# Kernel tuning notes

Measured on AMD Instinct MI355X. Metric: run time of the kernel, lower is better.

## Reference

```python
import jax, jax.numpy as jnp
import numpy as np

N, D, DR, DA = 50000, 128, 64, 64
R, A = 2000, 5000
L, H = 2, 2
E, E2, EA = 400000, 800000, 400000


def setup_inputs() -> dict:
    key = jax.random.key(0)
    ks = jax.random.split(key, 8)
    rng = np.random.default_rng(0)

    ee = np.stack([rng.integers(0, N, E), rng.integers(0, N, E)], 1)
    ee = ee[np.lexsort((ee[:, 1], ee[:, 0]))]            # sorted unique-ish ent-ent edges
    seg_id = np.repeat(np.arange(E), 2)                  # 2 relation rows per edge
    er_rel = rng.integers(0, R, E2)
    er_index = np.stack([np.repeat(ee[:, 0], 2), er_rel], 1)   # (node, rel) pairs
    ea_index = np.stack([rng.integers(0, N, EA), rng.integers(0, A, EA)], 1)
    ea_index = ea_index[np.lexsort((ea_index[:, 1], ea_index[:, 0]))]

    s192 = 1.0 / np.sqrt(192.0)
    s320 = 1.0 / np.sqrt(320.0)
    return {
        "ent_emb": jax.random.normal(ks[0], (N, D), jnp.float32) * 0.1,
        "rel_emb": jax.random.normal(ks[1], (R, DR), jnp.float32) * 0.1,
        "attr_emb": jax.random.normal(ks[2], (A, DA), jnp.float32) * 0.1,
        "w_r": jax.random.normal(ks[3], (192, 1), jnp.float32) * s192,
        "b_r": jnp.zeros((1,), jnp.float32),
        "w_a": jax.random.normal(ks[4], (192, 1), jnp.float32) * s192,
        "b_a": jnp.zeros((1,), jnp.float32),
        "ent_attn_w": jax.random.normal(ks[5], (L, H, 192, 1), jnp.float32) * s192,
        "ent_attn_b": jnp.zeros((L, H, 1), jnp.float32),
        "con_attn_w": jax.random.normal(ks[6], (L, H, 320, 1), jnp.float32) * s320,
        "con_attn_b": jnp.zeros((L, H, 1), jnp.float32),
        "ee_index": jnp.asarray(ee, jnp.int32),
        "seg_id": jnp.asarray(seg_id, jnp.int32),
        "er_rel": jnp.asarray(er_rel, jnp.int32),
        "er_index": jnp.asarray(er_index, jnp.int32),
        "ea_index": jnp.asarray(ea_index, jnp.int32),
    }


def _leaky(v):
    return jnp.where(v > 0, v, 0.3 * v)  # LeakyReLU(alpha=0.3)


def _seg_softmax(vals, seg, n):
    m = jax.ops.segment_max(vals, seg, num_segments=n)
    e = jnp.exp(vals - m[seg])
    s = jax.ops.segment_sum(e, seg, num_segments=n)
    return e / s[seg]


def _forward(ent_emb, rel_emb, attr_emb, w_r, b_r, w_a, b_a,
             eaw, eab, caw, cab, ee_index, seg_id, er_rel, er_index, ea_index):
    n, d = ent_emb.shape
    nl, nh = eaw.shape[0], eaw.shape[1]
    dh = d // nh
    ne = ee_index.shape[0]

    def concept(idx, emb, w, b):
        feat = jnp.concatenate([ent_emb[idx[:, 0]], emb[idx[:, 1]]], axis=1)
        a = _leaky(feat @ w + b).reshape(-1)
        p = _seg_softmax(a, idx[:, 0], n)                      # tf.sparse.softmax per row
        return jax.nn.relu(jax.ops.segment_sum(p[:, None] * emb[idx[:, 1]], idx[:, 0], num_segments=n))

    concept_rel = concept(er_index, rel_emb, w_r, b_r)         # (N, DR)
    concept_attr = concept(ea_index, attr_emb, w_a, b_a)       # (N, DA)

    row, col = ee_index[:, 0], ee_index[:, 1]
    # softmax over all-ones sparse adj == neighbor mean
    deg = jax.ops.segment_sum(jnp.ones((ne,), ent_emb.dtype), row, num_segments=n)
    x = jax.ops.segment_sum(ent_emb[col], row, num_segments=n) / jnp.maximum(deg, 1.0)[:, None]

    # segment_mean of relation embeddings over duplicate (h,t) edges
    cnt = jax.ops.segment_sum(jnp.ones((er_rel.shape[0],), ent_emb.dtype), seg_id, num_segments=ne)
    rels_mean = jax.ops.segment_sum(rel_emb[er_rel], seg_id, num_segments=ne) / jnp.maximum(cnt, 1.0)[:, None]

    # concept features per edge (same for every layer/head -> hoisted)
    con_feat = jnp.concatenate([concept_rel[row], concept_attr[row], rels_mean,
                                concept_rel[col], concept_attr[col]], axis=1)  # (E, 320)

    layer_outs = []
    for l in range(nl):
        x = jax.nn.relu(x)
        heads = x.reshape(n, nh, dh)
        outs = []
        for h in range(nh):
            xe = heads[:, h, :]
            nf = xe[col]
            ef = jnp.concatenate([xe[row], rels_mean, nf], axis=1)      # (E, 192)
            ea = _leaky(ef @ eaw[l, h] + eab[l, h]).reshape(-1)
            ca = _leaky(con_feat @ caw[l, h] + cab[l, h]).reshape(-1)
            p = jax.nn.softmax(ea * ca)         # tf.nn.softmax over all edge values
            p = _seg_softmax(p, row, n)          # then tf.sparse.softmax per row
            outs.append(jax.ops.segment_sum(p[:, None] * nf, row, num_segments=n))
        x = jnp.tanh(jnp.concatenate(outs, axis=1))
        layer_outs.append(x)

    grat_out = jnp.concatenate(layer_outs, axis=1)                     # (N, L*D)
    ent_out = jnp.concatenate([grat_out, concept_rel, concept_attr], axis=1)
    conc = jnp.concatenate([concept_rel, concept_attr], axis=1)
    return ent_out, conc


def reference(ent_emb, rel_emb, attr_emb, w_r, b_r, w_a, b_a,
              ent_attn_w, ent_attn_b, con_attn_w, con_attn_b,
              ee_index, seg_id, er_rel, er_index, ea_index):
    return _forward(ent_emb, rel_emb, attr_emb, w_r, b_r, w_a, b_a,
                    ent_attn_w, ent_attn_b, con_attn_w, con_attn_b,
                    ee_index, seg_id, er_rel, er_index, ea_index)
```

## Files before the change

### kernel.cpp

```cpp
#include <hip/hip_runtime.h>
#include <math.h>

#define NENT 50000
#define RREL 2000
#define AATT 5000
#define EE   400000
#define E2   800000
#define EAE  400000
#define PB   2048

__device__ __forceinline__ float leaky(float v){ return v > 0.f ? v : 0.3f * v; }

__device__ __forceinline__ float wave_sum(float v){
#pragma unroll
  for (int m = 32; m; m >>= 1) v += __shfl_xor(v, m);
  return v;
}
__device__ __forceinline__ float sum16(float v){
#pragma unroll
  for (int m = 1; m < 16; m <<= 1) v += __shfl_xor(v, m);
  return v;
}
__device__ __forceinline__ float max16(float v){
#pragma unroll
  for (int m = 1; m < 16; m <<= 1) v = fmaxf(v, __shfl_xor(v, m));
  return v;
}
__device__ __forceinline__ float sum8(float v){
#pragma unroll
  for (int m = 1; m < 8; m <<= 1) v += __shfl_xor(v, m);
  return v;
}

__device__ int lowb(const int* a, int n, int key){
  int lo = 0, hi = n;
  while (lo < hi){ int mid = (lo + hi) >> 1; if (a[2 * mid] < key) lo = mid + 1; else hi = mid; }
  return lo;
}

__global__ void k_ptr(const int* ee, const int* er, const int* ea,
                      int* pee, int* per, int* pea){
  int i = blockIdx.x * blockDim.x + threadIdx.x;
  if (i > NENT) return;
  pee[i] = lowb(ee, EE, i);
  per[i] = lowb(er, E2, i);
  pea[i] = lowb(ea, EAE, i);
}

__global__ void k_small(const float* rel_emb, const float* attr_emb,
                        const float* w_r, const float* w_a,
                        const float* eaw, const float* caw,
                        float* h_rel, float* h_attr, float4* HH0, float4* HH1){
  int t = blockIdx.x * blockDim.x + threadIdx.x;
  if (t < RREL){
    const float* e = rel_emb + (size_t)t * 64;
    float s = 0.f;
    for (int k = 0; k < 64; ++k) s += e[k] * w_r[128 + k];
    h_rel[t] = s;
    float hr[4], hc[4];
    for (int lh = 0; lh < 4; ++lh){
      float a = 0.f, c = 0.f;
      for (int k = 0; k < 64; ++k){
        a += e[k] * eaw[lh * 192 + 64 + k];
        c += e[k] * caw[lh * 320 + 128 + k];
      }
      hr[lh] = a; hc[lh] = c;
    }
    HH0[t] = make_float4(hr[0], hr[1], hc[0], hc[1]);
    HH1[t] = make_float4(hr[2], hr[3], hc[2], hc[3]);
  }
  if (t < AATT){
    const float* e = attr_emb + (size_t)t * 64;
    float s = 0.f;
    for (int k = 0; k < 64; ++k) s += e[k] * w_a[128 + k];
    h_attr[t] = s;
  }
}

__device__ float4 concept_g(float he, const float* h_tab, const int* idx,
                            int beg, int end, const float* emb, int p, int base){
  float m = -INFINITY, t = 0.f;
  for (int e = beg + p; e < end; e += 16){
    float v = leaky(he + h_tab[((const int2*)idx)[e].y]);
    float mn = fmaxf(m, v);
    t = t * __expf(m - mn) + __expf(v - mn);
    m = mn;
  }
  float M = max16(m);
  float z = sum16((t > 0.f) ? t * __expf(m - M) : 0.f);
  float invz = (z > 0.f) ? (1.f / z) : 0.f;
  float4 acc = {0.f, 0.f, 0.f, 0.f};
  for (int c0 = beg; c0 < end; c0 += 16){
    int e = c0 + p;
    int obj = 0; float wgt = 0.f;
    if (e < end){
      obj = ((const int2*)idx)[e].y;
      wgt = __expf(leaky(he + h_tab[obj]) - M) * invz;
    }
    int cnt = end - c0; if (cnt > 16) cnt = 16;
    for (int j = 0; j < cnt; ++j){
      int oj   = __shfl(obj, base | j);
      float wj = __shfl(wgt, base | j);
      float4 f = ((const float4*)(emb + (size_t)oj * 64))[p];
      acc.x = fmaf(wj, f.x, acc.x); acc.y = fmaf(wj, f.y, acc.y);
      acc.z = fmaf(wj, f.z, acc.z); acc.w = fmaf(wj, f.w, acc.w);
    }
  }
  acc.x = fmaxf(acc.x, 0.f); acc.y = fmaxf(acc.y, 0.f);
  acc.z = fmaxf(acc.z, 0.f); acc.w = fmaxf(acc.w, 0.f);
  return acc;
}

__global__ void k_phase1(const float* ent_emb, const float* rel_emb, const float* attr_emb,
                         const float* w_r, const float* b_r, const float* w_a, const float* b_a,
                         const float* eaw, const float* caw,
                         const int* er_idx, const int* ea_idx, const int* ee,
                         const int* per, const int* pea, const int* pee,
                         const float* h_rel, const float* h_attr,
                         float4* UA0, float4* VB0, float4* UA1, float4* VB1,
                         float* out){
  int tid = blockIdx.x * blockDim.x + threadIdx.x;
  int lane = threadIdx.x & 63;
  int p = lane & 15, g = lane >> 4, base = lane & 48;
  int w = (tid >> 6) * 4 + g;
  if (w >= NENT) return;
  const float4* erow = (const float4*)(ent_emb + (size_t)w * 128);
  float4 f0 = erow[2 * p], f1 = erow[2 * p + 1];
  const float4* wr4 = (const float4*)w_r;
  const float4* wa4 = (const float4*)w_a;
  float4 r0 = wr4[2 * p], r1 = wr4[2 * p + 1];
  float4 a0 = wa4[2 * p], a1 = wa4[2 * p + 1];
  float sr = f0.x*r0.x + f0.y*r0.y + f0.z*r0.z + f0.w*r0.w
           + f1.x*r1.x + f1.y*r1.y + f1.z*r1.z + f1.w*r1.w;
  float sa = f0.x*a0.x + f0.y*a0.y + f0.z*a0.z + f0.w*a0.w
           + f1.x*a1.x + f1.y*a1.y + f1.z*a1.z + f1.w*a1.w;
  float heR = sum16(sr) + b_r[0];
  float heA = sum16(sa) + b_a[0];
  float4 accR = concept_g(heR, h_rel, er_idx, per[w], per[w + 1], rel_emb, p, base);
  float4 accA = concept_g(heA, h_attr, ea_idx, pea[w], pea[w + 1], attr_emb, p, base);
  ((float4*)(out + (size_t)w * 384 + 256))[p] = accR;
  ((float4*)(out + (size_t)w * 384 + 320))[p] = accA;
  ((float4*)(out + (size_t)NENT * 384 + (size_t)w * 128))[p] = accR;
  ((float4*)(out + (size_t)NENT * 384 + (size_t)w * 128 + 64))[p] = accA;
  int beg = pee[w], end = pee[w + 1];
  float4 mx = {0.f,0.f,0.f,0.f}, my = {0.f,0.f,0.f,0.f};
  for (int c0 = beg; c0 < end; c0 += 16){
    int e = c0 + p;
    int col = (e < end) ? ((const int2*)ee)[e].y : 0;
    int cnt = end - c0; if (cnt > 16) cnt = 16;
    for (int j = 0; j < cnt; ++j){
      int cj = __shfl(col, base | j);
      const float4* r = (const float4*)(ent_emb + (size_t)cj * 128);
      float4 q0 = r[2 * p], q1 = r[2 * p + 1];
      mx.x += q0.x; mx.y += q0.y; mx.z += q0.z; mx.w += q0.w;
      my.x += q1.x; my.y += q1.y; my.z += q1.z; my.w += q1.w;
    }
  }
  float invd = 1.f / fmaxf((float)(end - beg), 1.f);
  mx.x *= invd; mx.y *= invd; mx.z *= invd; mx.w *= invd;
  my.x *= invd; my.y *= invd; my.z *= invd; my.w *= invd;
  ((float4*)(out + (size_t)w * 384 + 128))[2 * p]     = mx;
  ((float4*)(out + (size_t)w * 384 + 128))[2 * p + 1] = my;
#pragma unroll
  for (int lh = 0; lh < 4; ++lh){
    const float* cw = caw + lh * 320;
    float4 c0 = *(const float4*)(cw + 4 * p);
    float4 c1 = *(const float4*)(cw + 64 + 4 * p);
    float4 c2 = *(const float4*)(cw + 192 + 4 * p);
    float4 c3 = *(const float4*)(cw + 256 + 4 * p);
    float av = accR.x*c0.x + accR.y*c0.y + accR.z*c0.z + accR.w*c0.w
             + accA.x*c1.x + accA.y*c1.y + accA.z*c1.z + accA.w*c1.w;
    float bv = accR.x*c2.x + accR.y*c2.y + accR.z*c2.z + accR.w*c2.w
             + accA.x*c3.x + accA.y*c3.y + accA.z*c3.z + accA.w*c3.w;
    av = sum16(av); bv = sum16(bv);
    if (p == 0){
      float4* U = (lh < 2) ? UA0 : UA1;
      float4* V = (lh < 2) ? VB0 : VB1;
      ((float*)(U + w))[2 + (lh & 1)] = av;
      ((float*)(V + w))[2 + (lh & 1)] = bv;
    }
  }
  {
    int hh = p >> 3;
    int dbase = (8 * p) & 63;
    const float* wvp = eaw + hh * 192;
    float4 u0 = *(const float4*)(wvp + dbase);
    float4 u1 = *(const float4*)(wvp + dbase + 4);
    float4 q0 = *(const float4*)(wvp + 128 + dbase);
    float4 q1 = *(const float4*)(wvp + 128 + dbase + 4);
    float e0 = fmaxf(mx.x,0.f), e1 = fmaxf(mx.y,0.f), e2 = fmaxf(mx.z,0.f), e3 = fmaxf(mx.w,0.f);
    float e4 = fmaxf(my.x,0.f), e5 = fmaxf(my.y,0.f), e6 = fmaxf(my.z,0.f), e7 = fmaxf(my.w,0.f);
    float pu = e0*u0.x + e1*u0.y + e2*u0.z + e3*u0.w
             + e4*u1.x + e5*u1.y + e6*u1.z + e7*u1.w;
    float pv = e0*q0.x + e1*q0.y + e2*q0.z + e3*q0.w
             + e4*q1.x + e5*q1.y + e6*q1.z + e7*q1.w;
    pu = sum8(pu); pv = sum8(pv);
    if (p == 0 || p == 8){
      ((float*)(UA0 + w))[hh] = pu;
      ((float*)(VB0 + w))[hh] = pv;
    }
  }
}

__global__ void k_se(const int* ee, const int* err,
                     const float4* UA, const float4* VB, const float4* HH,
                     const float* eab_l, const float* cab_l,
                     float* s0, float* s1, float* partials){
  int e = blockIdx.x * blockDim.x + threadIdx.x;
  int tid = threadIdx.x;
  __shared__ float sm0[4], sm1[4];
  float ex0 = 0.f, ex1 = 0.f;
  if (e < EE){
    int2 rc = ((const int2*)ee)[e];
    int2 rr = ((const int2*)err)[e];
    float4 ua = UA[rc.x], vb = VB[rc.y], h1 = HH[rr.x], h2 = HH[rr.y];
    float ea0 = ua.x + 0.5f * (h1.x + h2.x) + vb.x + eab_l[0];
    float ca0 = ua.z + 0.5f * (h1.z + h2.z) + vb.z + cab_l[0];
    ex0 = __expf(leaky(ea0) * leaky(ca0));
    s0[e] = ex0;
    float ea1 = ua.y + 0.5f * (h1.y + h2.y) + vb.y + eab_l[1];
    float ca1 = ua.w + 0.5f * (h1.w + h2.w) + vb.w + cab_l[1];
    ex1 = __expf(leaky(ea1) * leaky(ca1));
    s1[e] = ex1;
  }
  float b0 = wave_sum(ex0), b1 = wave_sum(ex1);
  if ((tid & 63) == 0){ sm0[tid >> 6] = b0; sm1[tid >> 6] = b1; }
  __syncthreads();
  if (tid == 0)  partials[blockIdx.x]      = sm0[0] + sm0[1] + sm0[2] + sm0[3];
  if (tid == 64) partials[PB + blockIdx.x] = sm1[0] + sm1[1] + sm1[2] + sm1[3];
}

__global__ void k_final(const float* partials, float* scal, int nb){
  __shared__ float sm[1024];
  int tid = threadIdx.x;
  for (int h = 0; h < 2; ++h){
    float v = 0.f;
    for (int i = tid; i < nb; i += 1024) v += partials[h * PB + i];
    sm[tid] = v; __syncthreads();
    for (int s = 512; s; s >>= 1){
      if (tid < s) sm[tid] += sm[tid + s];
      __syncthreads();
    }
    if (tid == 0) scal[h] = sm[0];
    __syncthreads();
  }
}

__global__ void k_agg(const int* ee, const int* ptr, const float* s0, const float* s1,
                      const float* scal, const float* xsrc, float* outp, int ocol,
                      const float* eaw_next, float4* UAn, float4* VBn){
  int tid = blockIdx.x * blockDim.x + threadIdx.x;
  int lane = threadIdx.x & 63;
  int p = lane & 15, base = lane & 48;
  int w = (tid >> 6) * 4 + (lane >> 4);
  if (w >= NENT) return;
  int beg = ptr[w], end = ptr[w + 1];
  float invZ0 = 1.f / scal[0], invZ1 = 1.f / scal[1];
  float m0 = -INFINITY, m1 = -INFINITY, t0 = 0.f, t1 = 0.f;
  for (int e = beg + p; e < end; e += 16){
    float q0 = s0[e] * invZ0, q1 = s1[e] * invZ1;
    float n0 = fmaxf(m0, q0); t0 = t0 * __expf(m0 - n0) + __expf(q0 - n0); m0 = n0;
    float n1 = fmaxf(m1, q1); t1 = t1 * __expf(m1 - n1) + __expf(q1 - n1); m1 = n1;
  }
  float M0 = max16(m0), M1 = max16(m1);
  float z0 = sum16((t0 > 0.f) ? t0 * __expf(m0 - M0) : 0.f);
  float z1 = sum16((t1 > 0.f) ? t1 * __expf(m1 - M1) : 0.f);
  float iz0 = (z0 > 0.f) ? (1.f / z0) : 0.f;
  float iz1 = (z1 > 0.f) ? (1.f / z1) : 0.f;
  float4 a0 = {0.f,0.f,0.f,0.f}, a1 = {0.f,0.f,0.f,0.f};
  for (int c0 = beg; c0 < end; c0 += 16){
    int e = c0 + p;
    int col = 0; float w0 = 0.f, w1 = 0.f;
    if (e < end){
      col = ((const int2*)ee)[e].y;
      w0 = __expf(s0[e] * invZ0 - M0) * iz0;
      w1 = __expf(s1[e] * invZ1 - M1) * iz1;
    }
    int cnt = end - c0; if (cnt > 16) cnt = 16;
    for (int j = 0; j < cnt; ++j){
      int cj    = __shfl(col, base | j);
      float wj0 = __shfl(w0,  base | j);
      float wj1 = __shfl(w1,  base | j);
      const float4* r = (const float4*)(xsrc + (size_t)cj * 384);
      float4 f0 = r[2 * p], f1 = r[2 * p + 1];
      float ws = (p < 8) ? wj0 : wj1;
      a0.x = fmaf(ws, fmaxf(f0.x, 0.f), a0.x);
      a0.y = fmaf(ws, fmaxf(f0.y, 0.f), a0.y);
      a0.z = fmaf(ws, fmaxf(f0.z, 0.f), a0.z);
      a0.w = fmaf(ws, fmaxf(f0.w, 0.f), a0.w);
      a1.x = fmaf(ws, fmaxf(f1.x, 0.f), a1.x);
      a1.y = fmaf(ws, fmaxf(f1.y, 0.f), a1.y);
      a1.z = fmaf(ws, fmaxf(f1.z, 0.f), a1.z);
      a1.w = fmaf(ws, fmaxf(f1.w, 0.f), a1.w);
    }
  }
  float4 o0, o1;
  o0.x = tanhf(a0.x); o0.y = tanhf(a0.y); o0.z = tanhf(a0.z); o0.w = tanhf(a0.w);
  o1.x = tanhf(a1.x); o1.y = tanhf(a1.y); o1.z = tanhf(a1.z); o1.w = tanhf(a1.w);
  ((float4*)(outp + (size_t)w * 384 + ocol))[2 * p]     = o0;
  ((float4*)(outp + (size_t)w * 384 + ocol))[2 * p + 1] = o1;
  if (eaw_next){
    int hh = p >> 3;
    int dbase = (8 * p) & 63;
    const float* wvp = eaw_next + hh * 192;
    float4 u0 = *(const float4*)(wvp + dbase);
    float4 u1 = *(const float4*)(wvp + dbase + 4);
    float4 q0 = *(const float4*)(wvp + 128 + dbase);
    float4 q1 = *(const float4*)(wvp + 128 + dbase + 4);
    float e0 = fmaxf(o0.x,0.f), e1 = fmaxf(o0.y,0.f), e2 = fmaxf(o0.z,0.f), e3 = fmaxf(o0.w,0.f);
    float e4 = fmaxf(o1.x,0.f), e5 = fmaxf(o1.y,0.f), e6 = fmaxf(o1.z,0.f), e7 = fmaxf(o1.w,0.f);
    float pu = e0*u0.x + e1*u0.y + e2*u0.z + e3*u0.w
             + e4*u1.x + e5*u1.y + e6*u1.z + e7*u1.w;
    float pv = e0*q0.x + e1*q0.y + e2*q0.z + e3*q0.w
             + e4*q1.x + e5*q1.y + e6*q1.z + e7*q1.w;
    pu = sum8(pu); pv = sum8(pv);
    if (p == 0 || p == 8){
      ((float*)(UAn + w))[hh] = pu;
      ((float*)(VBn + w))[hh] = pv;
    }
  }
}

extern "C" void kernel_launch(void* const* d_in, const int* in_sizes, int n_in,
                              void* d_out, int out_size, void* d_ws, size_t ws_size,
                              hipStream_t stream){
  const float* ent_emb  = (const float*)d_in[0];
  const float* rel_emb  = (const float*)d_in[1];
  const float* attr_emb = (const float*)d_in[2];
  const float* w_r      = (const float*)d_in[3];
  const float* b_r      = (const float*)d_in[4];
  const float* w_a      = (const float*)d_in[5];
  const float* b_a      = (const float*)d_in[6];
  const float* eaw      = (const float*)d_in[7];
  const float* eab      = (const float*)d_in[8];
  const float* caw      = (const float*)d_in[9];
  const float* cab      = (const float*)d_in[10];
  const int*   ee       = (const int*)d_in[11];
  const int*   er_rel2  = (const int*)d_in[13];
  const int*   er_idx   = (const int*)d_in[14];
  const int*   ea_idx   = (const int*)d_in[15];
  float* out = (float*)d_out;

  int* pee = (int*)d_ws;
  int* per = pee + (NENT + 1);
  int* pea = per + (NENT + 1);
  float*  fbase = (float*)d_ws + 150004;
  float4* UA0 = (float4*)fbase;
  float4* VB0 = UA0 + NENT;
  float4* UA1 = VB0 + NENT;
  float4* VB1 = UA1 + NENT;
  float4* HH0 = VB1 + NENT;
  float4* HH1 = HH0 + RREL;
  float* s0      = (float*)(HH1 + RREL);
  float* s1      = s0 + EE;
  float* h_rel   = s1 + EE;
  float* h_attr  = h_rel + RREL;
  float* partials= h_attr + AATT;
  float* scal    = partials + 2 * PB;

  const int nb = (EE + 255) / 256;
  const int gq = (NENT + 15) / 16;

  k_ptr<<<(NENT + 1 + 255) / 256, 256, 0, stream>>>(ee, er_idx, ea_idx, pee, per, pea);
  k_small<<<(AATT + 255) / 256, 256, 0, stream>>>(rel_emb, attr_emb, w_r, w_a, eaw, caw,
                                                  h_rel, h_attr, HH0, HH1);
  k_phase1<<<gq, 256, 0, stream>>>(ent_emb, rel_emb, attr_emb, w_r, b_r, w_a, b_a,
                                   eaw, caw, er_idx, ea_idx, ee, per, pea, pee,
                                   h_rel, h_attr, UA0, VB0, UA1, VB1, out);
  k_se<<<nb, 256, 0, stream>>>(ee, er_rel2, UA0, VB0, HH0, eab, cab, s0, s1, partials);
  k_final<<<1, 1024, 0, stream>>>(partials, scal, nb);
  k_agg<<<gq, 256, 0, stream>>>(ee, pee, s0, s1, scal, out + 128, out, 0,
                                eaw + 2 * 192, UA1, VB1);
  k_se<<<nb, 256, 0, stream>>>(ee, er_rel2, UA1, VB1, HH1, eab + 2, cab + 2, s0, s1, partials);
  k_final<<<1, 1024, 0, stream>>>(partials, scal, nb);
  k_agg<<<gq, 256, 0, stream>>>(ee, pee, s0, s1, scal, out, out, 128,
                                (const float*)nullptr, (float4*)nullptr, (float4*)nullptr);
}
```

Before: 211.7 us.

## Precompute per-edge softmax exponentials and drop max-subtraction in segment softmax

The change moves the per-edge attention exponentials into separate edge-parallel kernels: entity scores are computed once per node, and the concept weights exp(leaky(...)) and the edge softmax exp(s/Z) are written to workspace. The aggregation kernels then only sum the precomputed weights, with no online max or rescaling, and gather rows with an unrolled, masked 4- or 8-wide loop instead of shuffle broadcasts. s0 and s1 are packed into a float2 array. The max-subtraction is dropped, which relies on the values being small enough not to overflow exp, and the change adds extra kernel launches and workspace traffic.

```diff
diff --git a/kernel.cpp b/kernel.cpp
--- a/kernel.cpp
+++ b/kernel.cpp
@@ -19,11 +19,6 @@
 __device__ __forceinline__ float sum16(float v){
 #pragma unroll
   for (int m = 1; m < 16; m <<= 1) v += __shfl_xor(v, m);
-  return v;
-}
-__device__ __forceinline__ float max16(float v){
-#pragma unroll
-  for (int m = 1; m < 16; m <<= 1) v = fmaxf(v, __shfl_xor(v, m));
   return v;
 }
 __device__ __forceinline__ float sum8(float v){
@@ -77,33 +72,45 @@
   }
 }
 
-__device__ float4 concept_g(float he, const float* h_tab, const int* idx,
-                            int beg, int end, const float* emb, int p, int base){
-  float m = -INFINITY, t = 0.f;
-  for (int e = beg + p; e < end; e += 16){
-    float v = leaky(he + h_tab[((const int2*)idx)[e].y]);
-    float mn = fmaxf(m, v);
-    t = t * __expf(m - mn) + __expf(v - mn);
-    m = mn;
-  }
-  float M = max16(m);
-  float z = sum16((t > 0.f) ? t * __expf(m - M) : 0.f);
-  float invz = (z > 0.f) ? (1.f / z) : 0.f;
+__global__ void k_ent_tab(const float* ent_emb, const float* w_r, const float* w_a,
+                          float* her, float* hea){
+  int w = (blockIdx.x * blockDim.x + threadIdx.x) >> 6;
+  int lane = threadIdx.x & 63;
+  if (w >= NENT) return;
+  float2 v = ((const float2*)(ent_emb + (size_t)w * 128))[lane];
+  float2 a = ((const float2*)w_r)[lane];
+  float2 b = ((const float2*)w_a)[lane];
+  float sr = wave_sum(v.x * a.x + v.y * a.y);
+  float sa = wave_sum(v.x * b.x + v.y * b.y);
+  if (lane == 0){ her[w] = sr; hea[w] = sa; }
+}
+
+__global__ void k_cw(const int* idx, int ne, const float* het, const float* h_tab,
+                     const float* bp, float* wout){
+  int e = blockIdx.x * blockDim.x + threadIdx.x;
+  if (e >= ne) return;
+  int2 rc = ((const int2*)idx)[e];
+  wout[e] = __expf(leaky(het[rc.x] + h_tab[rc.y] + bp[0]));
+}
+
+__device__ float4 concept_g(const float* wq, const int* idx, int beg, int end,
+                            const float* emb, int p){
+  float t = 0.f;
+  for (int e = beg + p; e < end; e += 16) t += wq[e];
+  t = sum16(t);
+  float invz = (t > 0.f) ? (1.f / t) : 0.f;
   float4 acc = {0.f, 0.f, 0.f, 0.f};
-  for (int c0 = beg; c0 < end; c0 += 16){
-    int e = c0 + p;
-    int obj = 0; float wgt = 0.f;
-    if (e < end){
-      obj = ((const int2*)idx)[e].y;
-      wgt = __expf(leaky(he + h_tab[obj]) - M) * invz;
-    }
-    int cnt = end - c0; if (cnt > 16) cnt = 16;
-    for (int j = 0; j < cnt; ++j){
-      int oj   = __shfl(obj, base | j);
-      float wj = __shfl(wgt, base | j);
-      float4 f = ((const float4*)(emb + (size_t)oj * 64))[p];
-      acc.x = fmaf(wj, f.x, acc.x); acc.y = fmaf(wj, f.y, acc.y);
-      acc.z = fmaf(wj, f.z, acc.z); acc.w = fmaf(wj, f.w, acc.w);
+  for (int c0 = beg; c0 < end; c0 += 8){
+    int cnt = end - c0; if (cnt > 8) cnt = 8;
+#pragma unroll
+    for (int j = 0; j < 8; ++j){
+      int e = c0 + ((j < cnt) ? j : 0);
+      float wgt = wq[e] * invz;
+      if (j >= cnt) wgt = 0.f;
+      int obj = ((const int2*)idx)[e].y;
+      float4 f = ((const float4*)(emb + (size_t)obj * 64))[p];
+      acc.x = fmaf(wgt, f.x, acc.x); acc.y = fmaf(wgt, f.y, acc.y);
+      acc.z = fmaf(wgt, f.z, acc.z); acc.w = fmaf(wgt, f.w, acc.w);
     }
   }
   acc.x = fmaxf(acc.x, 0.f); acc.y = fmaxf(acc.y, 0.f);
@@ -112,48 +119,38 @@
 }
 
 __global__ void k_phase1(const float* ent_emb, const float* rel_emb, const float* attr_emb,
-                         const float* w_r, const float* b_r, const float* w_a, const float* b_a,
                          const float* eaw, const float* caw,
                          const int* er_idx, const int* ea_idx, const int* ee,
                          const int* per, const int* pea, const int* pee,
-                         const float* h_rel, const float* h_attr,
+                         const float* wr, const float* wa,
                          float4* UA0, float4* VB0, float4* UA1, float4* VB1,
                          float* out){
   int tid = blockIdx.x * blockDim.x + threadIdx.x;
   int lane = threadIdx.x & 63;
-  int p = lane & 15, g = lane >> 4, base = lane & 48;
-  int w = (tid >> 6) * 4 + g;
+  int p = lane & 15;
+  int w = (tid >> 6) * 4 + (lane >> 4);
   if (w >= NENT) return;
-  const float4* erow = (const float4*)(ent_emb + (size_t)w * 128);
-  float4 f0 = erow[2 * p], f1 = erow[2 * p + 1];
-  const float4* wr4 = (const float4*)w_r;
-  const float4* wa4 = (const float4*)w_a;
-  float4 r0 = wr4[2 * p], r1 = wr4[2 * p + 1];
-  float4 a0 = wa4[2 * p], a1 = wa4[2 * p + 1];
-  float sr = f0.x*r0.x + f0.y*r0.y + f0.z*r0.z + f0.w*r0.w
-           + f1.x*r1.x + f1.y*r1.y + f1.z*r1.z + f1.w*r1.w;
-  float sa = f0.x*a0.x + f0.y*a0.y + f0.z*a0.z + f0.w*a0.w
-           + f1.x*a1.x + f1.y*a1.y + f1.z*a1.z + f1.w*a1.w;
-  float heR = sum16(sr) + b_r[0];
-  float heA = sum16(sa) + b_a[0];
-  float4 accR = concept_g(heR, h_rel, er_idx, per[w], per[w + 1], rel_emb, p, base);
-  float4 accA = concept_g(heA, h_attr, ea_idx, pea[w], pea[w + 1], attr_emb, p, base);
+  float4 accR = concept_g(wr, er_idx, per[w], per[w + 1], rel_emb, p);
+  float4 accA = concept_g(wa, ea_idx, pea[w], pea[w + 1], attr_emb, p);
   ((float4*)(out + (size_t)w * 384 + 256))[p] = accR;
   ((float4*)(out + (size_t)w * 384 + 320))[p] = accA;
   ((float4*)(out + (size_t)NENT * 384 + (size_t)w * 128))[p] = accR;
   ((float4*)(out + (size_t)NENT * 384 + (size_t)w * 128 + 64))[p] = accA;
   int beg = pee[w], end = pee[w + 1];
   float4 mx = {0.f,0.f,0.f,0.f}, my = {0.f,0.f,0.f,0.f};
-  for (int c0 = beg; c0 < end; c0 += 16){
-    int e = c0 + p;
-    int col = (e < end) ? ((const int2*)ee)[e].y : 0;
-    int cnt = end - c0; if (cnt > 16) cnt = 16;
-    for (int j = 0; j < cnt; ++j){
-      int cj = __shfl(col, base | j);
-      const float4* r = (const float4*)(ent_emb + (size_t)cj * 128);
+  for (int c0 = beg; c0 < end; c0 += 4){
+    int cnt = end - c0; if (cnt > 4) cnt = 4;
+#pragma unroll
+    for (int j = 0; j < 4; ++j){
+      int e = c0 + ((j < cnt) ? j : 0);
+      float msk = (j < cnt) ? 1.f : 0.f;
+      int ce = ((const int2*)ee)[e].y;
+      const float4* r = (const float4*)(ent_emb + (size_t)ce * 128);
       float4 q0 = r[2 * p], q1 = r[2 * p + 1];
-      mx.x += q0.x; mx.y += q0.y; mx.z += q0.z; mx.w += q0.w;
-      my.x += q1.x; my.y += q1.y; my.z += q1.z; my.w += q1.w;
+      mx.x = fmaf(msk, q0.x, mx.x); mx.y = fmaf(msk, q0.y, mx.y);
+      mx.z = fmaf(msk, q0.z, mx.z); mx.w = fmaf(msk, q0.w, mx.w);
+      my.x = fmaf(msk, q1.x, my.x); my.y = fmaf(msk, q1.y, my.y);
+      my.z = fmaf(msk, q1.z, my.z); my.w = fmaf(msk, q1.w, my.w);
     }
   }
   float invd = 1.f / fmaxf((float)(end - beg), 1.f);
@@ -205,7 +202,7 @@
 __global__ void k_se(const int* ee, const int* err,
                      const float4* UA, const float4* VB, const float4* HH,
                      const float* eab_l, const float* cab_l,
-                     float* s0, float* s1, float* partials){
+                     float2* s01, float* partials){
   int e = blockIdx.x * blockDim.x + threadIdx.x;
   int tid = threadIdx.x;
   __shared__ float sm0[4], sm1[4];
@@ -217,11 +214,10 @@
     float ea0 = ua.x + 0.5f * (h1.x + h2.x) + vb.x + eab_l[0];
     float ca0 = ua.z + 0.5f * (h1.z + h2.z) + vb.z + cab_l[0];
     ex0 = __expf(leaky(ea0) * leaky(ca0));
-    s0[e] = ex0;
     float ea1 = ua.y + 0.5f * (h1.y + h2.y) + vb.y + eab_l[1];
     float ca1 = ua.w + 0.5f * (h1.w + h2.w) + vb.w + cab_l[1];
     ex1 = __expf(leaky(ea1) * leaky(ca1));
-    s1[e] = ex1;
+    s01[e] = make_float2(ex0, ex1);
   }
   float b0 = wave_sum(ex0), b1 = wave_sum(ex1);
   if ((tid & 63) == 0){ sm0[tid >> 6] = b0; sm1[tid >> 6] = b1; }
@@ -246,44 +242,44 @@
   }
 }
 
-__global__ void k_agg(const int* ee, const int* ptr, const float* s0, const float* s1,
-                      const float* scal, const float* xsrc, float* outp, int ocol,
+__global__ void k_q(float2* s01, const float* scal){
+  int e = blockIdx.x * blockDim.x + threadIdx.x;
+  if (e >= EE) return;
+  float invZ0 = 1.f / scal[0], invZ1 = 1.f / scal[1];
+  float2 s = s01[e];
+  s01[e] = make_float2(__expf(s.x * invZ0), __expf(s.y * invZ1));
+}
+
+__global__ void k_agg(const int* ee, const int* ptr, const float2* q01,
+                      const float* xsrc, float* outp, int ocol,
                       const float* eaw_next, float4* UAn, float4* VBn){
   int tid = blockIdx.x * blockDim.x + threadIdx.x;
   int lane = threadIdx.x & 63;
-  int p = lane & 15, base = lane & 48;
+  int p = lane & 15;
   int w = (tid >> 6) * 4 + (lane >> 4);
   if (w >= NENT) return;
   int beg = ptr[w], end = ptr[w + 1];
-  float invZ0 = 1.f / scal[0], invZ1 = 1.f / scal[1];
-  float m0 = -INFINITY, m1 = -INFINITY, t0 = 0.f, t1 = 0.f;
+  float t0 = 0.f, t1 = 0.f;
   for (int e = beg + p; e < end; e += 16){
-    float q0 = s0[e] * invZ0, q1 = s1[e] * invZ1;
-    float n0 = fmaxf(m0, q0); t0 = t0 * __expf(m0 - n0) + __expf(q0 - n0); m0 = n0;
-    float n1 = fmaxf(m1, q1); t1 = t1 * __expf(m1 - n1) + __expf(q1 - n1); m1 = n1;
-  }
-  float M0 = max16(m0), M1 = max16(m1);
-  float z0 = sum16((t0 > 0.f) ? t0 * __expf(m0 - M0) : 0.f);
-  float z1 = sum16((t1 > 0.f) ? t1 * __expf(m1 - M1) : 0.f);
-  float iz0 = (z0 > 0.f) ? (1.f / z0) : 0.f;
-  float iz1 = (z1 > 0.f) ? (1.f / z1) : 0.f;
+    float2 q = q01[e];
+    t0 += q.x; t1 += q.y;
+  }
+  t0 = sum16(t0); t1 = sum16(t1);
+  float iz0 = (t0 > 0.f) ? (1.f / t0) : 0.f;
+  float iz1 = (t1 > 0.f) ? (1.f / t1) : 0.f;
+  float izs = (p < 8) ? iz0 : iz1;
   float4 a0 = {0.f,0.f,0.f,0.f}, a1 = {0.f,0.f,0.f,0.f};
-  for (int c0 = beg; c0 < end; c0 += 16){
-    int e = c0 + p;
-    int col = 0; float w0 = 0.f, w1 = 0.f;
-    if (e < end){
-      col = ((const int2*)ee)[e].y;
-      w0 = __expf(s0[e] * invZ0 - M0) * iz0;
-      w1 = __expf(s1[e] * invZ1 - M1) * iz1;
-    }
-    int cnt = end - c0; if (cnt > 16) cnt = 16;
-    for (int j = 0; j < cnt; ++j){
-      int cj    = __shfl(col, base | j);
-      float wj0 = __shfl(w0,  base | j);
-      float wj1 = __shfl(w1,  base | j);
+  for (int c0 = beg; c0 < end; c0 += 4){
+    int cnt = end - c0; if (cnt > 4) cnt = 4;
+#pragma unroll
+    for (int j = 0; j < 4; ++j){
+      int e = c0 + ((j < cnt) ? j : 0);
+      float2 q = q01[e];
+      float ws = ((p < 8) ? q.x : q.y) * izs;
+      if (j >= cnt) ws = 0.f;
+      int cj = ((const int2*)ee)[e].y;
       const float4* r = (const float4*)(xsrc + (size_t)cj * 384);
       float4 f0 = r[2 * p], f1 = r[2 * p + 1];
-      float ws = (p < 8) ? wj0 : wj1;
       a0.x = fmaf(ws, fmaxf(f0.x, 0.f), a0.x);
       a0.y = fmaf(ws, fmaxf(f0.y, 0.f), a0.y);
       a0.z = fmaf(ws, fmaxf(f0.z, 0.f), a0.z);
@@ -351,28 +347,37 @@
   float4* VB1 = UA1 + NENT;
   float4* HH0 = VB1 + NENT;
   float4* HH1 = HH0 + RREL;
-  float* s0      = (float*)(HH1 + RREL);
-  float* s1      = s0 + EE;
-  float* h_rel   = s1 + EE;
+  float* her     = (float*)(HH1 + RREL);
+  float* hea     = her + NENT;
+  float* h_rel   = hea + NENT;
   float* h_attr  = h_rel + RREL;
   float* partials= h_attr + AATT;
   float* scal    = partials + 2 * PB;
+  float* wr      = scal + 4;
+  float* wa      = wr + E2;
+  float2* s01    = (float2*)wr;
 
   const int nb = (EE + 255) / 256;
   const int gq = (NENT + 15) / 16;
+  const int gw = (NENT + 3) / 4;
 
   k_ptr<<<(NENT + 1 + 255) / 256, 256, 0, stream>>>(ee, er_idx, ea_idx, pee, per, pea);
   k_small<<<(AATT + 255) / 256, 256, 0, stream>>>(rel_emb, attr_emb, w_r, w_a, eaw, caw,
                                                   h_rel, h_attr, HH0, HH1);
-  k_phase1<<<gq, 256, 0, stream>>>(ent_emb, rel_emb, attr_emb, w_r, b_r, w_a, b_a,
-                                   eaw, caw, er_idx, ea_idx, ee, per, pea, pee,
-                                   h_rel, h_attr, UA0, VB0, UA1, VB1, out);
-  k_se<<<nb, 256, 0, stream>>>(ee, er_rel2, UA0, VB0, HH0, eab, cab, s0, s1, partials);
+  k_ent_tab<<<gw, 256, 0, stream>>>(ent_emb, w_r, w_a, her, hea);
+  k_cw<<<(E2 + 255) / 256, 256, 0, stream>>>(er_idx, E2, her, h_rel, b_r, wr);
+  k_cw<<<(EAE + 255) / 256, 256, 0, stream>>>(ea_idx, EAE, hea, h_attr, b_a, wa);
+  k_phase1<<<gq, 256, 0, stream>>>(ent_emb, rel_emb, attr_emb, eaw, caw,
+                                   er_idx, ea_idx, ee, per, pea, pee, wr, wa,
+                                   UA0, VB0, UA1, VB1, out);
+  k_se<<<nb, 256, 0, stream>>>(ee, er_rel2, UA0, VB0, HH0, eab, cab, s01, partials);
   k_final<<<1, 1024, 0, stream>>>(partials, scal, nb);
-  k_agg<<<gq, 256, 0, stream>>>(ee, pee, s0, s1, scal, out + 128, out, 0,
+  k_q<<<nb, 256, 0, stream>>>(s01, scal);
+  k_agg<<<gq, 256, 0, stream>>>(ee, pee, s01, out + 128, out, 0,
                                 eaw + 2 * 192, UA1, VB1);
-  k_se<<<nb, 256, 0, stream>>>(ee, er_rel2, UA1, VB1, HH1, eab + 2, cab + 2, s0, s1, partials);
+  k_se<<<nb, 256, 0, stream>>>(ee, er_rel2, UA1, VB1, HH1, eab + 2, cab + 2, s01, partials);
   k_final<<<1, 1024, 0, stream>>>(partials, scal, nb);
-  k_agg<<<gq, 256, 0, stream>>>(ee, pee, s0, s1, scal, out, out, 128,
+  k_q<<<nb, 256, 0, stream>>>(s01, scal);
+  k_agg<<<gq, 256, 0, stream>>>(ee, pee, s01, out, out, 128,
                                 (const float*)nullptr, (float4*)nullptr, (float4*)nullptr);
 }
```

New measurement: 211.3 us. About the same (-0.2%).
